# Performance work log

Hardware: AMD Instinct MI355X
Metric: run time of the kernel (lower is better)

## Reference

```python
import jax, jax.numpy as jnp
import numpy as np
import math

EPS = 1e-5  # BatchNorm eps; eval mode with running_mean=0, running_var=1


def maxpool(x, k, p):
    return jax.lax.reduce_window(x, -jnp.inf, jax.lax.max,
                                 (1, 1, k, k), (1, 1, 1, 1),
                                 ((0, 0), (0, 0), (p, p), (p, p)))


def conv1x1(x, w, b=None):
    # x: [B,Cin,H,W], w: [Cout,Cin]
    y = jnp.einsum('oi,bihw->bohw', w, x)
    if b is not None:
        y = y + b[None, :, None, None]
    return y


def bn_eval(x, g, b):
    scale = g / jnp.sqrt(1.0 + EPS)
    return x * scale[None, :, None, None] + b[None, :, None, None]


def setup_inputs() -> dict:
    B, C, H, W = 2, 64, 80, 80
    c1, c2, c3 = 21, 21, 22
    ch = 32  # C//2
    ks = jax.random.split(jax.random.key(0), 16)
    s = 0.05
    inp = {
        'x': jax.random.normal(ks[0], (B, C, H, W), jnp.float32),
        'q1_w': jax.random.normal(ks[1], (c1, c1), jnp.float32) * s,
        'q1_g': jnp.ones((c1,), jnp.float32),
        'q1_b': jnp.zeros((c1,), jnp.float32),
        'q2_w': jax.random.normal(ks[2], (c2, c2), jnp.float32) * s,
        'q2_g': jnp.ones((c2,), jnp.float32),
        'q2_b': jnp.zeros((c2,), jnp.float32),
        'q3_w': jax.random.normal(ks[3], (c3, c3), jnp.float32) * s,
        'q3_g': jnp.ones((c3,), jnp.float32),
        'q3_b': jnp.zeros((c3,), jnp.float32),
        'k_hf_w': jax.random.normal(ks[4], (ch, C), jnp.float32) * s,
        'k_hf_b': jnp.zeros((ch,), jnp.float32),
        'k_lf_w': jax.random.normal(ks[5], (C - ch, C), jnp.float32) * s,
        'k_lf_b': jnp.zeros((C - ch,), jnp.float32),
        'k_fuse_w': jax.random.normal(ks[6], (C, C), jnp.float32) * s,
        'k_fuse_b': jnp.zeros((C,), jnp.float32),
        'v_bn_g': jnp.ones((C,), jnp.float32),
        'v_bn_b': jnp.zeros((C,), jnp.float32),
        'v_w': jax.random.normal(ks[7], (C, C), jnp.float32) * s,
        'v_b': jnp.zeros((C,), jnp.float32),
        'out_w': jax.random.normal(ks[8], (C, C), jnp.float32) * s,
        'out_b': jnp.zeros((C,), jnp.float32),
    }
    return inp


def reference(x, q1_w, q1_g, q1_b, q2_w, q2_g, q2_b, q3_w, q3_g, q3_b,
              k_hf_w, k_hf_b, k_lf_w, k_lf_b, k_fuse_w, k_fuse_b,
              v_bn_g, v_bn_b, v_w, v_b, out_w, out_b):
    B, C, H, W = x.shape
    N = H * W
    c1 = q1_w.shape[0]
    c2 = q2_w.shape[0]
    # Q: ThreeGroupConvQ (split -> 1x1 conv (no bias) -> BN -> ReLU -> concat)
    x1, x2, x3 = jnp.split(x, [c1, c1 + c2], axis=1)
    y1 = jax.nn.relu(bn_eval(conv1x1(x1, q1_w), q1_g, q1_b))
    y2 = jax.nn.relu(bn_eval(conv1x1(x2, q2_w), q2_g, q2_b))
    y3 = jax.nn.relu(bn_eval(conv1x1(x3, q3_w), q3_g, q3_b))
    Q = jnp.concatenate([y1, y2, y3], axis=1)
    # K: ThermalStructureExtractor
    p3 = maxpool(x, 3, 1)
    p5 = maxpool(x, 5, 2)
    low = (p3 + p5) * 0.5
    high = conv1x1(x - low, k_hf_w, k_hf_b)
    lowp = conv1x1(low, k_lf_w, k_lf_b)
    K = conv1x1(jnp.concatenate([high, lowp], axis=1), k_fuse_w, k_fuse_b)
    # V: BN -> 1x1 conv
    V = conv1x1(bn_eval(x, v_bn_g, v_bn_b), v_w, v_b)
    # attention over N = H*W spatial tokens, channel features
    Qc = Q.reshape(B, C, N)
    Kc = K.reshape(B, C, N)
    Vc = V.reshape(B, C, N)
    attn = jax.nn.softmax(
        jnp.einsum('bcn,bcm->bnm', Qc, Kc) / math.sqrt(C), axis=-1)  # [B,N,N]
    out = jnp.einsum('bnm,bcm->bcn', attn, Vc).reshape(B, C, H, W)
    return conv1x1(out, out_w, out_b) + x
```

## Files before the change

### kernel.cpp

```cpp
#include <hip/hip_runtime.h>
#include <hip/hip_bf16.h>


#define BATCH 2
#define CH 64
#define HH 80
#define WW 80
#define NN 6400
#define NT 100
#define KS 10
#define KTPS (NT/KS)
#define EPSV 1e-5f
#define NEGBIG (-1e30f)
#define QP 72
#define LOG2E8 0.18033688f
#define VSP 65

typedef __hip_bfloat16 bf16;
typedef __attribute__((ext_vector_type(8))) short short8;
typedef __attribute__((ext_vector_type(4))) float f4;
#define MFMA16 __builtin_amdgcn_mfma_f32_16x16x32_bf16

__device__ __forceinline__ float b2f(bf16 v){ return __bfloat162float(v); }
__device__ __forceinline__ bf16 f2b(float v){ return __float2bfloat16(v); }
__device__ __forceinline__ ushort f2bu(float v){ return ((__hip_bfloat16_raw)__float2bfloat16(v)).x; }
__device__ __forceinline__ float bu2f(ushort u){
  union { unsigned int i; float f; } w; w.i = ((unsigned int)u) << 16; return w.f;
}
__device__ __forceinline__ unsigned pkbf(float a, float b){
  union { __hip_bfloat162 h2; unsigned u; } cv;
  cv.h2 = __float22bfloat162_rn(make_float2(a, b));
  return cv.u;
}
__device__ __forceinline__ float fexp2(float x){
#if __has_builtin(__builtin_amdgcn_exp2f)
  return __builtin_amdgcn_exp2f(x);
#else
  return exp2f(x);
#endif
}

#define OFF_BIAS 0
#define OFF_WH_B 768
#define OFF_LOW_B (768 + 32768)
#define OFF_Q_B   (OFF_LOW_B + BATCH*CH*NN*2)
#define OFF_K_B   (OFF_Q_B   + BATCH*CH*NN*2)
#define OFF_V_B   (OFF_K_B   + BATCH*CH*NN*2)
#define OFF_P_B   (OFF_V_B   + BATCH*CH*NN*2)
#define OFF_ML_B  (OFF_P_B   + BATCH*NT*KS*4096*2)

__global__ __launch_bounds__(256) void setup_fold(
    const float* __restrict__ q1w, const float* __restrict__ q1g, const float* __restrict__ q1b,
    const float* __restrict__ q2w, const float* __restrict__ q2g, const float* __restrict__ q2b,
    const float* __restrict__ q3w, const float* __restrict__ q3g, const float* __restrict__ q3b,
    const float* __restrict__ khw, const float* __restrict__ khb,
    const float* __restrict__ klw, const float* __restrict__ klb,
    const float* __restrict__ kfw, const float* __restrict__ kfb,
    const float* __restrict__ vg,  const float* __restrict__ vbnb,
    const float* __restrict__ vw,  const float* __restrict__ vb,
    const float* __restrict__ outw,
    float* __restrict__ biasf, bf16* __restrict__ wh)
{
  __shared__ __align__(16) float skf[4096];
  __shared__ __align__(16) float skh[2048];
  __shared__ __align__(16) float skl[2048];
  __shared__ __align__(16) float sow[4096];
  __shared__ __align__(16) float svw[4096];
  __shared__ float sbv[64];

  int tid = threadIdx.x;
  int blk = blockIdx.x;
  #pragma unroll
  for (int i = 0; i < 4; ++i) {
    *(float4*)&skf[(i*256 + tid)*4] = *(const float4*)&kfw[(i*256 + tid)*4];
    *(float4*)&sow[(i*256 + tid)*4] = *(const float4*)&outw[(i*256 + tid)*4];
    *(float4*)&svw[(i*256 + tid)*4] = *(const float4*)&vw[(i*256 + tid)*4];
  }
  #pragma unroll
  for (int i = 0; i < 2; ++i) {
    *(float4*)&skh[(i*256 + tid)*4] = *(const float4*)&khw[(i*256 + tid)*4];
    *(float4*)&skl[(i*256 + tid)*4] = *(const float4*)&klw[(i*256 + tid)*4];
  }
  __syncthreads();

  float rs = rsqrtf(1.0f + EPSV);
  if (tid < 64) {
    int j = tid;
    float bvo = vb[j];
    for (int ci2 = 0; ci2 < 64; ++ci2) bvo += svw[j*64 + ci2] * vbnb[ci2];
    sbv[j] = bvo;
  }

  bf16* wq   = wh;
  bf16* wvp  = wh + 4096;
  bf16* wa1  = wh + 8192;
  bf16* wa2m = wh + 12288;

  int t = blk*256 + tid;
  int ci = t & 63, co = t >> 6;
  int o = ci*64 + co;

  float w = 0.f, g;
  if (co < 21)      { g = q1g[co];    w = (ci < 21)              ? q1w[co*21 + ci]            : 0.f; }
  else if (co < 42) { g = q2g[co-21]; w = (ci >= 21 && ci < 42)  ? q2w[(co-21)*21 + (ci-21)]  : 0.f; }
  else              { g = q3g[co-42]; w = (ci >= 42)             ? q3w[(co-42)*22 + (ci-42)]  : 0.f; }
  wq[o] = f2b(w * g * rs * LOG2E8);

  float a1 = 0.f, a2 = 0.f;
  #pragma unroll
  for (int j = 0; j < 32; ++j) {
    a1 += skf[co*64 + j]      * skh[j*64 + ci];
    a2 += skf[co*64 + 32 + j] * skl[j*64 + ci];
  }
  wa1[o]  = f2b(a1);
  wa2m[o] = f2b(a2 - a1);

  float av = 0.f;
  #pragma unroll
  for (int j = 0; j < 64; ++j)
    av += sow[co*64 + j] * svw[j*64 + ci];
  wvp[o] = f2b(av * vg[ci] * rs);

  if (blk == 0 && tid < 64) {
    int c2 = tid;
    float bq;
    if (c2 < 21)      bq = q1b[c2];
    else if (c2 < 42) bq = q2b[c2-21];
    else              bq = q3b[c2-42];
    biasf[c2] = bq * LOG2E8;
    float bk = kfb[c2];
    #pragma unroll
    for (int j = 0; j < 32; ++j) {
      bk += skf[c2*64 + j]      * khb[j];
      bk += skf[c2*64 + 32 + j] * klb[j];
    }
    biasf[64 + c2] = bk;
    float bvp = 0.f;
    #pragma unroll
    for (int j = 0; j < 64; ++j) bvp += sow[c2*64 + j] * sbv[j];
    biasf[128 + c2] = bvp;
  }
}

__global__ __launch_bounds__(256) void pool_low(const float* __restrict__ x,
                                                bf16* __restrict__ lowg)
{
  int t4 = (blockIdx.x*256 + threadIdx.x)*4;
  int bc = t4 / NN; int n = t4 % NN;
  int h = n / WW, w0 = n % WW;
  const float* p = x + bc*NN;
  float m5[4], m3[4];
  #pragma unroll
  for (int j=0;j<4;++j){ m5[j]=NEGBIG; m3[j]=NEGBIG; }
  #pragma unroll
  for (int dh = -2; dh <= 2; ++dh) {
    int hh = h + dh; if (hh < 0 || hh >= HH) continue;
    float r[12];
    const float* row = p + hh*WW;
    if (w0 >= 4)      { float4 a = *(const float4*)&row[w0-4]; r[0]=a.x;r[1]=a.y;r[2]=a.z;r[3]=a.w; }
    else              { r[0]=NEGBIG;r[1]=NEGBIG;r[2]=NEGBIG;r[3]=NEGBIG; }
    { float4 a = *(const float4*)&row[w0]; r[4]=a.x;r[5]=a.y;r[6]=a.z;r[7]=a.w; }
    if (w0 + 7 < WW)  { float4 a = *(const float4*)&row[w0+4]; r[8]=a.x;r[9]=a.y;r[10]=a.z;r[11]=a.w; }
    else              { r[8]=NEGBIG;r[9]=NEGBIG;r[10]=NEGBIG;r[11]=NEGBIG; }
    bool in3 = (dh >= -1 && dh <= 1);
    #pragma unroll
    for (int j=0;j<4;++j) {
      float v3 = fmaxf(fmaxf(r[3+j], r[4+j]), r[5+j]);
      float v5 = fmaxf(fmaxf(r[2+j], v3), r[6+j]);
      m5[j] = fmaxf(m5[j], v5);
      if (in3) m3[j] = fmaxf(m3[j], v3);
    }
  }
  ushort4 o;
  o.x = f2bu(0.5f*(m3[0]+m5[0]));
  o.y = f2bu(0.5f*(m3[1]+m5[1]));
  o.z = f2bu(0.5f*(m3[2]+m5[2]));
  o.w = f2bu(0.5f*(m3[3]+m5[3]));
  *(ushort4*)&lowg[t4] = o;
}

__global__ __launch_bounds__(256) void qkv_kernel(
    const float* __restrict__ x, const float* __restrict__ biasf,
    const bf16* __restrict__ wh, const bf16* __restrict__ lowg,
    bf16* __restrict__ qgT, bf16* __restrict__ kgT, bf16* __restrict__ vgc)
{
  __shared__ __align__(16) float xs[64*32];
  __shared__ __align__(16) float lows[64*32];
  __shared__ __align__(16) bf16  wbuf[16384];
  __shared__ ushort vs[64*VSP];
  __shared__ float bias[192];

  int tid = threadIdx.x;
  int blk = blockIdx.x;
  int b = blk / (NT*2);
  int rem = blk % (NT*2);
  int tile = rem >> 1, half = rem & 1;
  int n0 = tile*64 + half*32;

  #pragma unroll
  for (int i = 0; i < 8; ++i) {
    int e = i*256 + tid; int c = e >> 5, p = e & 31;
    xs[c*32 + p]   = x[(b*CH + c)*NN + n0 + p];
    lows[c*32 + p] = b2f(lowg[(b*CH + c)*NN + n0 + p]);
  }
  #pragma unroll
  for (int i = 0; i < 16; ++i)
    ((uint2*)wbuf)[i*256 + tid] = ((const uint2*)wh)[i*256 + tid];
  if (tid < 192) bias[tid] = biasf[tid];
  __syncthreads();

  int co = tid & 63, pg = tid >> 6;
  const bf16* wq   = wbuf;
  const bf16* wvp  = wbuf + 4096;
  const bf16* wa1  = wbuf + 8192;
  const bf16* wa2m = wbuf + 12288;

  {
    float bq = bias[co];
    float4 a0 = make_float4(bq,bq,bq,bq), a1v = a0;
    for (int ci = 0; ci < 64; ++ci) {
      float wv = b2f(wq[ci*64 + co]);
      float4 x0 = *(const float4*)&xs[ci*32 + pg*8];
      float4 x1 = *(const float4*)&xs[ci*32 + pg*8 + 4];
      a0.x += wv*x0.x; a0.y += wv*x0.y; a0.z += wv*x0.z; a0.w += wv*x0.w;
      a1v.x += wv*x1.x; a1v.y += wv*x1.y; a1v.z += wv*x1.z; a1v.w += wv*x1.w;
    }
    float q8[8] = {a0.x,a0.y,a0.z,a0.w,a1v.x,a1v.y,a1v.z,a1v.w};
    #pragma unroll
    for (int j=0;j<8;++j)
      qgT[(size_t)(b*NN + n0 + pg*8 + j)*64 + co] = f2b(fmaxf(q8[j], 0.f));
  }
  {
    float bv = bias[128 + co];
    float4 a0 = make_float4(bv,bv,bv,bv), a1v = a0;
    for (int ci = 0; ci < 64; ++ci) {
      float wv = b2f(wvp[ci*64 + co]);
      float4 x0 = *(const float4*)&xs[ci*32 + pg*8];
      float4 x1 = *(const float4*)&xs[ci*32 + pg*8 + 4];
      a0.x += wv*x0.x; a0.y += wv*x0.y; a0.z += wv*x0.z; a0.w += wv*x0.w;
      a1v.x += wv*x1.x; a1v.y += wv*x1.y; a1v.z += wv*x1.z; a1v.w += wv*x1.w;
    }
    float v8[8] = {a0.x,a0.y,a0.z,a0.w,a1v.x,a1v.y,a1v.z,a1v.w};
    #pragma unroll
    for (int j=0;j<8;++j)
      vs[co*VSP + pg*8 + j] = f2bu(v8[j]);
  }
  __syncthreads();
  {
    int c = tid >> 2, cb = (tid & 3)*8;
    ushort u[8];
    #pragma unroll
    for (int j=0;j<8;++j) u[j] = vs[c*VSP + cb + j];
    uint4 pk;
    pk.x = (uint)u[0] | ((uint)u[1] << 16);
    pk.y = (uint)u[2] | ((uint)u[3] << 16);
    pk.z = (uint)u[4] | ((uint)u[5] << 16);
    pk.w = (uint)u[6] | ((uint)u[7] << 16);
    *(uint4*)&vgc[(size_t)(b*CH + c)*NN + n0 + cb] = pk;
  }
  {
    float bk = bias[64 + co];
    float4 a0 = make_float4(bk,bk,bk,bk), a1v = a0;
    for (int ci = 0; ci < 64; ++ci) {
      float w1 = b2f(wa1[ci*64 + co]);
      float w2 = b2f(wa2m[ci*64 + co]);
      float4 x0 = *(const float4*)&xs[ci*32 + pg*8];
      float4 x1 = *(const float4*)&xs[ci*32 + pg*8 + 4];
      float4 l0 = *(const float4*)&lows[ci*32 + pg*8];
      float4 l1 = *(const float4*)&lows[ci*32 + pg*8 + 4];
      a0.x += w1*x0.x + w2*l0.x; a0.y += w1*x0.y + w2*l0.y;
      a0.z += w1*x0.z + w2*l0.z; a0.w += w1*x0.w + w2*l0.w;
      a1v.x += w1*x1.x + w2*l1.x; a1v.y += w1*x1.y + w2*l1.y;
      a1v.z += w1*x1.z + w2*l1.z; a1v.w += w1*x1.w + w2*l1.w;
    }
    float k8[8] = {a0.x,a0.y,a0.z,a0.w,a1v.x,a1v.y,a1v.z,a1v.w};
    #pragma unroll
    for (int j=0;j<8;++j)
      kgT[(size_t)(b*NN + n0 + pg*8 + j)*64 + co] = f2b(k8[j]);
  }
}

__global__ __launch_bounds__(256) void attn_partial(
    const bf16* __restrict__ qgT, const bf16* __restrict__ kgT, const bf16* __restrict__ vgc,
    ushort* __restrict__ part, float* __restrict__ pml)
{
  __shared__ __align__(16) char smem[27648];
  __shared__ float lred[256];
  bf16* Qld = (bf16*)smem;
  bf16* Pld = (bf16*)smem;
  bf16* Kld = (bf16*)(smem + 9216);
  bf16* Vld = (bf16*)(smem + 18432);

  int tid = threadIdx.x;
  int blk = blockIdx.x;
  int b = blk / (NT*KS);
  int rem = blk % (NT*KS);
  int tile = rem / KS, split = rem % KS;
  int n0 = tile*64;
  int wv = tid >> 6, lane = tid & 63, ln = lane & 15, quad = lane >> 4;
  int arow = (wv*16 + ln)*QP;

  #pragma unroll
  for (int i = 0; i < 4; ++i) {
    int f = (i*256 + tid)*4; int n = f >> 6, c = f & 63;
    *(uint2*)&Qld[n*QP + c] = *(const uint2*)&qgT[(size_t)(b*NN + n0 + n)*64 + c];
  }
  __syncthreads();
  short8 bq[4][2];
  #pragma unroll
  for (int nt = 0; nt < 4; ++nt) {
    bq[nt][0] = *(const short8*)&Qld[(nt*16 + ln)*QP + quad*8];
    bq[nt][1] = *(const short8*)&Qld[(nt*16 + ln)*QP + 32 + quad*8];
  }

  f4 accO[4];
  float lacc[4];
  #pragma unroll
  for (int t=0;t<4;++t) accO[t] = (f4){0.f,0.f,0.f,0.f};
  #pragma unroll
  for (int nt=0;nt<4;++nt) lacc[nt] = 0.f;

  uint2 kreg[4], vreg[4];
  int mbase = split*KTPS*64;
  #pragma unroll
  for (int i = 0; i < 4; ++i) {
    int f = (i*256 + tid)*4; int rr = f >> 6, cc = f & 63;
    kreg[i] = *(const uint2*)&kgT[(size_t)(b*NN + mbase + rr)*64 + cc];
    vreg[i] = *(const uint2*)&vgc[(size_t)(b*CH + rr)*NN + mbase + cc];
  }

  for (int kt = 0; kt < KTPS; ++kt) {
    __syncthreads();
    #pragma unroll
    for (int i = 0; i < 4; ++i) {
      int f = (i*256 + tid)*4; int rr = f >> 6, cc = f & 63;
      *(uint2*)&Kld[rr*QP + cc] = kreg[i];
      *(uint2*)&Vld[rr*QP + cc] = vreg[i];
    }
    __syncthreads();
    if (kt + 1 < KTPS) {
      int m0 = mbase + (kt+1)*64;
      #pragma unroll
      for (int i = 0; i < 4; ++i) {
        int f = (i*256 + tid)*4; int rr = f >> 6, cc = f & 63;
        kreg[i] = *(const uint2*)&kgT[(size_t)(b*NN + m0 + rr)*64 + cc];
        vreg[i] = *(const uint2*)&vgc[(size_t)(b*CH + rr)*NN + m0 + cc];
      }
    }

    short8 ak0 = *(const short8*)&Kld[arow + quad*8];
    short8 ak1 = *(const short8*)&Kld[arow + 32 + quad*8];
    f4 accS[4];
    #pragma unroll
    for (int nt = 0; nt < 4; ++nt) {
      f4 z = (f4){0.f,0.f,0.f,0.f};
      z = MFMA16(ak0, bq[nt][0], z, 0, 0, 0);
      accS[nt] = MFMA16(ak1, bq[nt][1], z, 0, 0, 0);
    }
    #pragma unroll
    for (int nt = 0; nt < 4; ++nt) {
      float p0 = fexp2(accS[nt][0]), p1 = fexp2(accS[nt][1]);
      float p2 = fexp2(accS[nt][2]), p3 = fexp2(accS[nt][3]);
      lacc[nt] += (p0 + p1) + (p2 + p3);
      uint2 pk;
      pk.x = pkbf(p0, p1);
      pk.y = pkbf(p2, p3);
      *(uint2*)&Pld[(nt*16 + ln)*QP + wv*16 + quad*4] = pk;
    }
    __syncthreads();

    short8 ap0 = *(const short8*)&Pld[arow + quad*8];
    short8 ap1 = *(const short8*)&Pld[arow + 32 + quad*8];
    #pragma unroll
    for (int t = 0; t < 4; ++t) {
      short8 bv0 = *(const short8*)&Vld[(t*16+ln)*QP + quad*8];
      short8 bv1 = *(const short8*)&Vld[(t*16+ln)*QP + 32 + quad*8];
      accO[t] = MFMA16(ap0, bv0, accO[t], 0, 0, 0);
      accO[t] = MFMA16(ap1, bv1, accO[t], 0, 0, 0);
    }
  }

  size_t pbase = ((size_t)(b*NT + tile)*KS + split)*4096;
  ushort* pp = part + pbase;
  #pragma unroll
  for (int t = 0; t < 4; ++t) {
    uint2 pk;
    pk.x = pkbf(accO[t][0], accO[t][1]);
    pk.y = pkbf(accO[t][2], accO[t][3]);
    *(uint2*)&pp[(t*16 + ln)*64 + wv*16 + quad*4] = pk;
  }
  #pragma unroll
  for (int nt = 0; nt < 4; ++nt) {
    float s = lacc[nt];
    s += __shfl_xor(s, 16);
    s += __shfl_xor(s, 32);
    if (quad == 0) lred[wv*64 + nt*16 + ln] = s;
  }
  __syncthreads();
  if (tid < 64) {
    size_t mlb = ((size_t)(b*NT + tile)*KS + split)*64;
    pml[mlb + tid] = (lred[tid] + lred[64 + tid]) + (lred[128 + tid] + lred[192 + tid]);
  }
}

__global__ __launch_bounds__(256) void attn_reduce(
    const ushort* __restrict__ part, const float* __restrict__ pml,
    const float* __restrict__ x, const float* __restrict__ outb,
    float* __restrict__ out)
{
  __shared__ float linv[64];
  __shared__ float ob[64];

  int tid = threadIdx.x;
  int blk = blockIdx.x;
  int b = blk / NT, tile = blk % NT;
  size_t base = (size_t)(b*NT + tile)*KS;

  if (tid < 64) {
    float l = 0.f;
    #pragma unroll
    for (int s=0;s<KS;++s) l += pml[(base+s)*64 + tid];
    linv[tid] = 1.0f / l;
    ob[tid] = outb[tid];
  }
  __syncthreads();

  #pragma unroll
  for (int j = 0; j < 4; ++j) {
    int idx = j*256 + tid;
    int c = idx >> 4, q = idx & 15;
    float a0=0.f, a1=0.f, a2=0.f, a3=0.f;
    #pragma unroll
    for (int s = 0; s < KS; ++s) {
      uint2 v = *(const uint2*)&part[(base+s)*4096 + (size_t)c*64 + q*4];
      a0 += bu2f((ushort)(v.x & 0xffff)); a1 += bu2f((ushort)(v.x >> 16));
      a2 += bu2f((ushort)(v.y & 0xffff)); a3 += bu2f((ushort)(v.y >> 16));
    }
    int nl = q*4;
    size_t gidx = (size_t)(b*CH + c)*NN + tile*64 + nl;
    float4 xv = *(const float4*)&x[gidx];
    float bc = ob[c];
    float4 o;
    o.x = a0*linv[nl+0] + bc + xv.x;
    o.y = a1*linv[nl+1] + bc + xv.y;
    o.z = a2*linv[nl+2] + bc + xv.z;
    o.w = a3*linv[nl+3] + bc + xv.w;
    *(float4*)&out[gidx] = o;
  }
}

extern "C" void kernel_launch(void* const* d_in, const int* in_sizes, int n_in,
                              void* d_out, int out_size, void* d_ws, size_t ws_size,
                              hipStream_t stream) {
  const float* x    = (const float*)d_in[0];
  const float* q1w  = (const float*)d_in[1];
  const float* q1g  = (const float*)d_in[2];
  const float* q1b  = (const float*)d_in[3];
  const float* q2w  = (const float*)d_in[4];
  const float* q2g  = (const float*)d_in[5];
  const float* q2b  = (const float*)d_in[6];
  const float* q3w  = (const float*)d_in[7];
  const float* q3g  = (const float*)d_in[8];
  const float* q3b  = (const float*)d_in[9];
  const float* khw  = (const float*)d_in[10];
  const float* khb  = (const float*)d_in[11];
  const float* klw  = (const float*)d_in[12];
  const float* klb  = (const float*)d_in[13];
  const float* kfw  = (const float*)d_in[14];
  const float* kfb  = (const float*)d_in[15];
  const float* vbg  = (const float*)d_in[16];
  const float* vbb  = (const float*)d_in[17];
  const float* vw   = (const float*)d_in[18];
  const float* vb   = (const float*)d_in[19];
  const float* outw = (const float*)d_in[20];
  const float* outb = (const float*)d_in[21];

  char*   wsb  = (char*)d_ws;
  float*  biasf= (float*)(wsb + OFF_BIAS);
  bf16*   wh   = (bf16*)(wsb + OFF_WH_B);
  bf16*   lowg = (bf16*)(wsb + OFF_LOW_B);
  bf16*   qgT  = (bf16*)(wsb + OFF_Q_B);
  bf16*   kgT  = (bf16*)(wsb + OFF_K_B);
  bf16*   vgc  = (bf16*)(wsb + OFF_V_B);
  ushort* part = (ushort*)(wsb + OFF_P_B);
  float*  pml  = (float*)(wsb + OFF_ML_B);

  hipLaunchKernelGGL(setup_fold, dim3(16), dim3(256), 0, stream,
                     q1w,q1g,q1b,q2w,q2g,q2b,q3w,q3g,q3b,
                     khw,khb,klw,klb,kfw,kfb,vbg,vbb,vw,vb,outw, biasf, wh);
  hipLaunchKernelGGL(pool_low, dim3(BATCH*CH*NN/1024), dim3(256), 0, stream, x, lowg);
  hipLaunchKernelGGL(qkv_kernel, dim3(BATCH*NT*2), dim3(256), 0, stream,
                     x, biasf, wh, lowg, qgT, kgT, vgc);
  hipLaunchKernelGGL(attn_partial, dim3(BATCH*NT*KS), dim3(256), 0, stream,
                     qgT, kgT, vgc, part, pml);
  hipLaunchKernelGGL(attn_reduce, dim3(BATCH*NT), dim3(256), 0, stream,
                     part, pml, x, outb, (float*)d_out);
}
```

Measured before the change: 172.1 us.

## Double-buffer attention LDS tiles with XOR swizzle and load K directly to registers

Restructures the attn_partial inner loop. K fragments are now read straight from global memory into MFMA operand registers instead of being staged through shared memory. The P and V tiles are double-buffered in LDS, which removes two of the three barriers per key tile. Padded rows are replaced by an XOR-swizzled 128-byte row layout with 16-byte vector loads and stores, meant to avoid bank conflicts. The trade-offs are uncoalesced per-lane global K reads and a larger shared memory footprint.

```diff
diff --git a/kernel.cpp b/kernel.cpp
--- a/kernel.cpp
+++ b/kernel.cpp
@@ -12,7 +12,6 @@
 #define KTPS (NT/KS)
 #define EPSV 1e-5f
 #define NEGBIG (-1e30f)
-#define QP 72
 #define LOG2E8 0.18033688f
 #define VSP 65
 
@@ -38,6 +37,9 @@
 #else
   return exp2f(x);
 #endif
+}
+__device__ __forceinline__ int swz(int row, int colb){
+  return row*128 + (colb ^ ((row & 7) << 4));
 }
 
 #define OFF_BIAS 0
@@ -284,12 +286,8 @@
     const bf16* __restrict__ qgT, const bf16* __restrict__ kgT, const bf16* __restrict__ vgc,
     ushort* __restrict__ part, float* __restrict__ pml)
 {
-  __shared__ __align__(16) char smem[27648];
+  __shared__ __align__(16) char smem[32768];
   __shared__ float lred[256];
-  bf16* Qld = (bf16*)smem;
-  bf16* Pld = (bf16*)smem;
-  bf16* Kld = (bf16*)(smem + 9216);
-  bf16* Vld = (bf16*)(smem + 18432);
 
   int tid = threadIdx.x;
   int blk = blockIdx.x;
@@ -298,20 +296,31 @@
   int tile = rem / KS, split = rem % KS;
   int n0 = tile*64;
   int wv = tid >> 6, lane = tid & 63, ln = lane & 15, quad = lane >> 4;
-  int arow = (wv*16 + ln)*QP;
-
-  #pragma unroll
-  for (int i = 0; i < 4; ++i) {
-    int f = (i*256 + tid)*4; int n = f >> 6, c = f & 63;
-    *(uint2*)&Qld[n*QP + c] = *(const uint2*)&qgT[(size_t)(b*NN + n0 + n)*64 + c];
+  int mbase = split*KTPS*64;
+
+  #pragma unroll
+  for (int i = 0; i < 2; ++i) {
+    int f = (i*256 + tid)*8; int n = f >> 6, c = f & 63;
+    uint4 q4 = *(const uint4*)&qgT[(size_t)(b*NN + n0 + n)*64 + c];
+    *(uint4*)(smem + swz(n, c*2)) = q4;
   }
   __syncthreads();
   short8 bq[4][2];
   #pragma unroll
   for (int nt = 0; nt < 4; ++nt) {
-    bq[nt][0] = *(const short8*)&Qld[(nt*16 + ln)*QP + quad*8];
-    bq[nt][1] = *(const short8*)&Qld[(nt*16 + ln)*QP + 32 + quad*8];
-  }
+    bq[nt][0] = *(const short8*)(smem + swz(nt*16 + ln, quad*16));
+    bq[nt][1] = *(const short8*)(smem + swz(nt*16 + ln, 64 + quad*16));
+  }
+  #pragma unroll
+  for (int i = 0; i < 2; ++i) {
+    int f = (i*256 + tid)*8; int rr = f >> 6, cc = f & 63;
+    uint4 v4 = *(const uint4*)&vgc[(size_t)(b*CH + rr)*NN + mbase + cc];
+    *(uint4*)(smem + 16384 + swz(rr, cc*2)) = v4;
+  }
+  const bf16* kb = kgT + (size_t)(b*NN + mbase + wv*16 + ln)*64;
+  short8 ak0 = *(const short8*)&kb[quad*8];
+  short8 ak1 = *(const short8*)&kb[32 + quad*8];
+  __syncthreads();
 
   f4 accO[4];
   float lacc[4];
@@ -320,36 +329,22 @@
   #pragma unroll
   for (int nt=0;nt<4;++nt) lacc[nt] = 0.f;
 
-  uint2 kreg[4], vreg[4];
-  int mbase = split*KTPS*64;
-  #pragma unroll
-  for (int i = 0; i < 4; ++i) {
-    int f = (i*256 + tid)*4; int rr = f >> 6, cc = f & 63;
-    kreg[i] = *(const uint2*)&kgT[(size_t)(b*NN + mbase + rr)*64 + cc];
-    vreg[i] = *(const uint2*)&vgc[(size_t)(b*CH + rr)*NN + mbase + cc];
-  }
-
+  uint4 vreg[2];
+  short8 an0, an1;
   for (int kt = 0; kt < KTPS; ++kt) {
-    __syncthreads();
-    #pragma unroll
-    for (int i = 0; i < 4; ++i) {
-      int f = (i*256 + tid)*4; int rr = f >> 6, cc = f & 63;
-      *(uint2*)&Kld[rr*QP + cc] = kreg[i];
-      *(uint2*)&Vld[rr*QP + cc] = vreg[i];
-    }
-    __syncthreads();
+    int po = (kt & 1) * 8192;
+    int vo = 16384 + (kt & 1) * 8192;
     if (kt + 1 < KTPS) {
-      int m0 = mbase + (kt+1)*64;
+      int m1 = mbase + (kt+1)*64;
       #pragma unroll
-      for (int i = 0; i < 4; ++i) {
-        int f = (i*256 + tid)*4; int rr = f >> 6, cc = f & 63;
-        kreg[i] = *(const uint2*)&kgT[(size_t)(b*NN + m0 + rr)*64 + cc];
-        vreg[i] = *(const uint2*)&vgc[(size_t)(b*CH + rr)*NN + m0 + cc];
+      for (int i = 0; i < 2; ++i) {
+        int f = (i*256 + tid)*8; int rr = f >> 6, cc = f & 63;
+        vreg[i] = *(const uint4*)&vgc[(size_t)(b*CH + rr)*NN + m1 + cc];
       }
-    }
-
-    short8 ak0 = *(const short8*)&Kld[arow + quad*8];
-    short8 ak1 = *(const short8*)&Kld[arow + 32 + quad*8];
+      an0 = *(const short8*)&kb[(size_t)(kt+1)*4096 + quad*8];
+      an1 = *(const short8*)&kb[(size_t)(kt+1)*4096 + 32 + quad*8];
+    }
+
     f4 accS[4];
     #pragma unroll
     for (int nt = 0; nt < 4; ++nt) {
@@ -365,18 +360,27 @@
       uint2 pk;
       pk.x = pkbf(p0, p1);
       pk.y = pkbf(p2, p3);
-      *(uint2*)&Pld[(nt*16 + ln)*QP + wv*16 + quad*4] = pk;
+      *(uint2*)(smem + po + swz(nt*16 + ln, wv*32 + quad*8)) = pk;
     }
     __syncthreads();
 
-    short8 ap0 = *(const short8*)&Pld[arow + quad*8];
-    short8 ap1 = *(const short8*)&Pld[arow + 32 + quad*8];
+    short8 ap0 = *(const short8*)(smem + po + swz(wv*16 + ln, quad*16));
+    short8 ap1 = *(const short8*)(smem + po + swz(wv*16 + ln, 64 + quad*16));
     #pragma unroll
     for (int t = 0; t < 4; ++t) {
-      short8 bv0 = *(const short8*)&Vld[(t*16+ln)*QP + quad*8];
-      short8 bv1 = *(const short8*)&Vld[(t*16+ln)*QP + 32 + quad*8];
+      short8 bv0 = *(const short8*)(smem + vo + swz(t*16 + ln, quad*16));
+      short8 bv1 = *(const short8*)(smem + vo + swz(t*16 + ln, 64 + quad*16));
       accO[t] = MFMA16(ap0, bv0, accO[t], 0, 0, 0);
       accO[t] = MFMA16(ap1, bv1, accO[t], 0, 0, 0);
+    }
+    if (kt + 1 < KTPS) {
+      int vn = 16384 + ((kt+1) & 1) * 8192;
+      #pragma unroll
+      for (int i = 0; i < 2; ++i) {
+        int f = (i*256 + tid)*8; int rr = f >> 6, cc = f & 63;
+        *(uint4*)(smem + vn + swz(rr, cc*2)) = vreg[i];
+      }
+      ak0 = an0; ak1 = an1;
     }
   }
 
```

Measured after the change: 182.8 us. +6.2%, slower.
